# Kernel tuning notes

Measured on AMD Instinct MI355X. Metric: run time of the kernel, lower is better.

## Reference

```python
import jax, jax.numpy as jnp
import numpy as np

N_HEAD = 16
ROPE_BASE = 10000.0


def _make_rope(max_seq, half_dim):
    inv_freq = 1.0 / (ROPE_BASE ** (np.arange(0, half_dim, dtype=np.float32) / half_dim))
    t = np.arange(max_seq, dtype=np.float32)
    freqs = np.outer(t, inv_freq)  # [T, half_dim]
    return jnp.asarray(np.cos(freqs)), jnp.asarray(np.sin(freqs))


def setup_inputs() -> dict:
    key = jax.random.key(0)
    k1, k2, k3 = jax.random.split(key, 3)
    B, T, C = 4, 2048, 2048
    D = C // N_HEAD
    x = jax.random.normal(k1, (B, T, C), dtype=jnp.float32)
    # torch Linear weight [out,in]; stored transposed so y = x @ W
    wqkv = jax.random.normal(k2, (C, 3 * C), dtype=jnp.float32) * (C ** -0.5)
    wo = jax.random.normal(k3, (C, C), dtype=jnp.float32) * (C ** -0.5)
    rope_cos, rope_sin = _make_rope(T, D // 2)
    return {"x": x, "wqkv": wqkv, "wo": wo, "rope_cos": rope_cos, "rope_sin": rope_sin}


def _apply_rope(t, cos, sin):
    # t: [B, T, H, D]; cos/sin: [T, D/2]
    B, T, H, D = t.shape
    tr = t.reshape(B, T, H, D // 2, 2)
    xr, xi = tr[..., 0], tr[..., 1]
    c = cos[:T][None, :, None, :]
    s = sin[:T][None, :, None, :]
    out_r = xr * c - xi * s
    out_i = xr * s + xi * c
    return jnp.stack([out_r, out_i], axis=-1).reshape(B, T, H, D)


def reference(x, wqkv, wo, rope_cos, rope_sin):
    B, T, C = x.shape
    H = N_HEAD
    D = C // H
    qkv = x @ wqkv  # [B, T, 3C]
    q, k, v = jnp.split(qkv, 3, axis=-1)
    q = _apply_rope(q.reshape(B, T, H, D), rope_cos, rope_sin)
    k = _apply_rope(k.reshape(B, T, H, D), rope_cos, rope_sin)
    v = v.reshape(B, T, H, D)
    scale = D ** -0.5
    scores = jnp.einsum('bqhd,bkhd->bhqk', q, k) * scale  # [B, H, T, T]
    causal = jnp.tril(jnp.ones((T, T), dtype=bool))
    scores = jnp.where(causal[None, None], scores, jnp.finfo(scores.dtype).min)
    attn = jax.nn.softmax(scores, axis=-1)
    y = jnp.einsum('bhqk,bkhd->bqhd', attn, v).reshape(B, T, C)
    return y @ wo
```

## Files before the change

### kernel.cpp

```cpp
#include <hip/hip_runtime.h>
#include <hip/hip_bf16.h>

typedef __attribute__((ext_vector_type(8))) __bf16 bf16x8;
typedef __attribute__((ext_vector_type(4))) float f32x4;
typedef __attribute__((ext_vector_type(4))) unsigned short us4;

__device__ __forceinline__ unsigned short f2bf(float f) {
    unsigned u = __float_as_uint(f);
    u += 0x7FFFu + ((u >> 16) & 1u);
    return (unsigned short)(u >> 16);
}

__device__ __forceinline__ void gload16(const void* g, void* l) {
    __builtin_amdgcn_global_load_lds(
        (const __attribute__((address_space(1))) unsigned int*)g,
        (__attribute__((address_space(3))) unsigned int*)l,
        16, 0, 0);
}

__global__ void cvt_f32_bf16(const float* __restrict__ in, unsigned short* __restrict__ out, int n4) {
    int i = blockIdx.x * blockDim.x + threadIdx.x;
    if (i >= n4) return;
    float4 v = ((const float4*)in)[i];
    us4 r = { f2bf(v.x), f2bf(v.y), f2bf(v.z), f2bf(v.w) };
    ((us4*)out)[i] = r;
}

__global__ void tcvt(const float* __restrict__ in, unsigned short* __restrict__ out, int R, int C) {
    __shared__ float tile[32][33];
    int tx = threadIdx.x & 31, ty = threadIdx.x >> 5;
    int c0 = blockIdx.x * 32, r0 = blockIdx.y * 32;
    #pragma unroll
    for (int i = 0; i < 32; i += 8)
        tile[ty + i][tx] = in[(size_t)(r0 + ty + i) * C + c0 + tx];
    __syncthreads();
    #pragma unroll
    for (int i = 0; i < 32; i += 8)
        out[(size_t)(c0 + ty + i) * R + r0 + tx] = f2bf(tile[tx][ty + i]);
}

#define MF(af, bf, fi, ni) acc[fi][ni] = __builtin_amdgcn_mfma_f32_16x16x32_bf16(af, bf, acc[fi][ni], 0, 0, 0)
#define LOADA(p, off) do { a0 = *(const bf16x8*)((p)+(off)); a1 = *(const bf16x8*)((p)+(off)+1024); \
                           a2 = *(const bf16x8*)((p)+(off)+2048); a3 = *(const bf16x8*)((p)+(off)+3072); } while(0)
#define LOADA2(p, off) do { a4 = *(const bf16x8*)((p)+(off)); a5 = *(const bf16x8*)((p)+(off)+1024); \
                            a6 = *(const bf16x8*)((p)+(off)+2048); a7 = *(const bf16x8*)((p)+(off)+3072); } while(0)
#define LOADB(p) do { b0 = *(const bf16x8*)(p); b1 = *(const bf16x8*)((p)+1024); \
                      b2 = *(const bf16x8*)((p)+2048); b3 = *(const bf16x8*)((p)+3072); } while(0)
#define MFMA32() do { \
    MF(a0,b0,0,0); MF(a0,b1,0,1); MF(a0,b2,0,2); MF(a0,b3,0,3); \
    MF(a1,b0,1,0); MF(a1,b1,1,1); MF(a1,b2,1,2); MF(a1,b3,1,3); \
    MF(a2,b0,2,0); MF(a2,b1,2,1); MF(a2,b2,2,2); MF(a2,b3,2,3); \
    MF(a3,b0,3,0); MF(a3,b1,3,1); MF(a3,b2,3,2); MF(a3,b3,3,3); \
    MF(a4,b0,4,0); MF(a4,b1,4,1); MF(a4,b2,4,2); MF(a4,b3,4,3); \
    MF(a5,b0,5,0); MF(a5,b1,5,1); MF(a5,b2,5,2); MF(a5,b3,5,3); \
    MF(a6,b0,6,0); MF(a6,b1,6,1); MF(a6,b2,6,2); MF(a6,b3,6,3); \
    MF(a7,b0,7,0); MF(a7,b1,7,1); MF(a7,b2,7,2); MF(a7,b3,7,3); } while(0)
#define STG(gb, lp, buf, kkk, kt) do { \
    size_t ko = (size_t)(kt) * 128 + (kkk) * 64; \
    char* lpp = (lp) + (buf) * 32768 + (kkk) * 16384; \
    gload16((gb) + sR0 + ko, lpp + dst0); \
    gload16((gb) + sR1 + ko, lpp + dst1); } while (0)
#define PHASE_SYNC() do { \
    __builtin_amdgcn_s_barrier(); \
    asm volatile("s_waitcnt lgkmcnt(0)" ::: "memory"); \
    __builtin_amdgcn_sched_barrier(0); } while (0)

template <int MODE>
__global__ __launch_bounds__(512) void gemm8p(
    const unsigned short* __restrict__ A, const unsigned short* __restrict__ Bt,
    int M, int N, int K, float* __restrict__ Cf,
    unsigned short* __restrict__ qp, unsigned short* __restrict__ kp,
    unsigned short* __restrict__ vTp,
    const float* __restrict__ ropeC, const float* __restrict__ ropeS,
    int cby, int cbx)
{
    __shared__ unsigned short lA[2][2][8192];
    __shared__ unsigned short lB[2][2][8192];
    const int tid = threadIdx.x;
    const int lane = tid & 63, wid = tid >> 6;
    const int ln15 = lane & 15, hig = lane >> 4;
    const int wr = wid >> 2, wc = wid & 3;

    int nwg = gridDim.x * gridDim.y;
    int flat = blockIdx.y * gridDim.x + blockIdx.x;
    int bx, by;
    if ((nwg & 7) == 0) {
        int c = flat & 7, local = flat >> 3;
        int chunkCols = gridDim.x / cbx;
        by = (c / chunkCols) * cby + local / cbx;
        bx = (c % chunkCols) * cbx + local % cbx;
    } else {
        bx = flat % gridDim.x; by = flat / gridDim.x;
    }
    const int mbase = by * 256, nbase = bx * 256;
    const size_t Kb = (size_t)K * 2;

    const char* Ag = (const char*)A + (size_t)mbase * Kb;
    const char* Bg = (const char*)Bt + (size_t)nbase * Kb;
    char* lAc = (char*)&lA[0][0][0];
    char* lBc = (char*)&lB[0][0][0];

    const int srow = tid >> 2;
    const int gsrc = (tid & 3) ^ (((tid >> 5) & 1) << 1);
    const size_t sR0 = (size_t)srow * Kb + gsrc * 16;
    const size_t sR1 = (size_t)(srow + 128) * Kb + gsrc * 16;
    const int dst0 = tid * 16, dst1 = (tid + 512) * 16;

    const int colOff = (hig * 16) ^ (((ln15 >> 3) & 1) << 5);
    const int aRow = (wr * 128 + ln15) * 64 + colOff;
    const int bRow = (wc * 64 + ln15) * 64 + colOff;

    f32x4 acc[8][4] = {};
    const int T = K >> 6;

    STG(Ag, lAc, 0, 0, 0);
    STG(Bg, lBc, 0, 0, 0);
    STG(Ag, lAc, 0, 1, 0);
    STG(Bg, lBc, 0, 1, 0);
    asm volatile("s_waitcnt vmcnt(4)" ::: "memory");
    __builtin_amdgcn_s_barrier();

    for (int t = 0; t < T; t++) {
        const int cur = t & 1, nxt = cur ^ 1;
        const char* pa0 = lAc + cur * 32768 + aRow;
        const char* pb0 = lBc + cur * 32768 + bRow;
        const char* pa1 = pa0 + 16384;
        const char* pb1 = pb0 + 16384;
        const bool more = (t + 1 < T);
        bf16x8 a0, a1, a2, a3, a4, a5, a6, a7, b0, b1, b2, b3;

        LOADA(pa0, 0);
        LOADA2(pa0, 4096);
        LOADB(pb0);
        if (more) { STG(Ag, lAc, nxt, 0, t + 1); STG(Bg, lBc, nxt, 0, t + 1); }
        asm volatile("s_waitcnt lgkmcnt(8)" ::: "memory");
        if (more) asm volatile("s_waitcnt vmcnt(4)" ::: "memory");
        else      asm volatile("s_waitcnt vmcnt(0)" ::: "memory");
        PHASE_SYNC();
        __builtin_amdgcn_s_setprio(1);
        MFMA32();
        __builtin_amdgcn_s_setprio(0);
        __builtin_amdgcn_s_barrier();

        LOADA(pa1, 0);
        LOADA2(pa1, 4096);
        LOADB(pb1);
        if (more) {
            STG(Ag, lAc, nxt, 1, t + 1);
            STG(Bg, lBc, nxt, 1, t + 1);
            asm volatile("s_waitcnt lgkmcnt(8)" ::: "memory");
            asm volatile("s_waitcnt vmcnt(4)" ::: "memory");
        }
        PHASE_SYNC();
        __builtin_amdgcn_s_setprio(1);
        MFMA32();
        __builtin_amdgcn_s_setprio(0);
        __builtin_amdgcn_s_barrier();
    }

    if (MODE == 0) {
        #pragma unroll
        for (int fg = 0; fg < 8; fg++)
            #pragma unroll
            for (int n = 0; n < 4; n++)
                #pragma unroll
                for (int j = 0; j < 4; j++) {
                    int m = mbase + wr * 128 + fg * 16 + hig * 4 + j;
                    int col = nbase + wc * 64 + n * 16 + ln15;
                    Cf[(size_t)m * N + col] = acc[fg][n][j];
                }
    } else {
        const int colb = nbase + wc * 64;
        const int sec = colb >> 11;
        if (sec < 2) {
            unsigned short* dst = (sec == 0) ? qp : kp;
            const float scale = (sec == 0) ? 0.08838834764831845f : 1.0f;
            #pragma unroll
            for (int fg = 0; fg < 8; fg++)
                #pragma unroll
                for (int n = 0; n < 4; n++) {
                    int within = (colb & 2047) + n * 16 + ln15;
                    int h = within >> 7, d = within & 127, pidx = d >> 1;
                    #pragma unroll
                    for (int j = 0; j < 4; j++) {
                        int m = mbase + wr * 128 + fg * 16 + hig * 4 + j;
                        int b = m >> 11, tq = m & 2047;
                        float v = acc[fg][n][j];
                        float pv = __shfl_xor(v, 1);
                        float c = ropeC[tq * 64 + pidx], s = ropeS[tq * 64 + pidx];
                        float o = (d & 1) ? fmaf(pv, s, v * c) : fmaf(-pv, s, v * c);
                        o *= scale;
                        dst[((size_t)((b << 4) + h) * 2048 + tq) * 128 + d] = f2bf(o);
                    }
                }
        } else {
            #pragma unroll
            for (int fg = 0; fg < 8; fg++)
                #pragma unroll
                for (int n = 0; n < 4; n++) {
                    int within = (colb & 2047) + n * 16 + ln15;
                    int h = within >> 7, d = within & 127;
                    int m0 = mbase + wr * 128 + fg * 16 + hig * 4;
                    int b = m0 >> 11, t0 = m0 & 2047;
                    us4 pk = { f2bf(acc[fg][n][0]), f2bf(acc[fg][n][1]),
                               f2bf(acc[fg][n][2]), f2bf(acc[fg][n][3]) };
                    *(us4*)(vTp + ((size_t)((b << 4) + h) * 128 + d) * 2048 + t0) = pk;
                }
        }
    }
}

__global__ __launch_bounds__(256, 2) void attn_fwd(
    const unsigned short* __restrict__ q, const unsigned short* __restrict__ k,
    const unsigned short* __restrict__ vT, unsigned short* __restrict__ outp)
{
    __shared__ unsigned short lK[2][64 * 128];
    __shared__ unsigned short lV[2][128 * 64];
    __shared__ unsigned short lP[4 * 32 * 64];
    const int tid = threadIdx.x;
    const int lane = tid & 63, wid = tid >> 6;
    const int ln15 = lane & 15, hig = lane >> 4, hi8 = hig * 8;
    const int bh = blockIdx.x;

    const char* qg = (const char*)(q + (size_t)bh * 2048 * 128);
    const char* kg = (const char*)(k + (size_t)bh * 2048 * 128);
    const char* vg = (const char*)(vT + (size_t)bh * 128 * 2048);
    char* lKc = (char*)&lK[0][0];
    char* lVc = (char*)&lV[0][0];
    char* lPc = (char*)lP + wid * (32 * 64 * 2);
    const int b = bh >> 4, h = bh & 15;

    for (int rep = 0; rep < 2; rep++) {
        const int qt = rep == 0 ? (int)blockIdx.y : 15 - (int)blockIdx.y;
        const int qbase = qt * 128;
        const int qw = qbase + wid * 32;

        bf16x8 qf[2][4];
        #pragma unroll
        for (int mt = 0; mt < 2; mt++)
            #pragma unroll
            for (int ks = 0; ks < 4; ks++)
                qf[mt][ks] = *(const bf16x8*)(qg + ((size_t)(qw + mt * 16 + ln15) * 128 + ks * 32 + hi8) * 2);

        f32x4 o[2][8] = {};
        float mreg[2] = { -1e30f, -1e30f };
        float lreg[2] = { 0.f, 0.f };

        auto stageKV = [&](int bf, int kv0) {
            #pragma unroll
            for (int i = 0; i < 4; i++) {
                int slot = tid + i * 256;
                int row = slot >> 4, c = (slot & 15) * 16;
                gload16(kg + (size_t)(kv0 + row) * 256 + (c ^ ((row & 7) << 4)),
                        lKc + bf * 16384 + slot * 16);
            }
            #pragma unroll
            for (int i = 0; i < 4; i++) {
                int slot = tid + i * 256;
                int d = slot >> 3, c = (slot & 7) * 16;
                gload16(vg + (size_t)d * 4096 + (size_t)kv0 * 2 + (c ^ ((d & 7) << 4)),
                        lVc + bf * 16384 + slot * 16);
            }
        };

        const int ntiles = (qbase >> 6) + 2;
        stageKV(0, 0);
        if (ntiles > 1) stageKV(1, 64);

        for (int it = 0; it < ntiles; it++) {
            const int kv0 = it * 64;
            const int buf = it & 1;
            if (it + 1 < ntiles) asm volatile("s_waitcnt vmcnt(8)" ::: "memory");
            else                 asm volatile("s_waitcnt vmcnt(0)" ::: "memory");
            __builtin_amdgcn_s_barrier();

            if (kv0 <= qw + 31) {
                const char* lKb = lKc + buf * 16384;
                const char* lVb = lVc + buf * 16384;

                f32x4 s[2][4] = {};
                #pragma unroll
                for (int ks = 0; ks < 4; ks++) {
                    bf16x8 kf[4];
                    #pragma unroll
                    for (int nt = 0; nt < 4; nt++) {
                        int row = nt * 16 + ln15;
                        kf[nt] = *(const bf16x8*)(lKb + row * 256 + (((ks * 32 + hi8) * 2) ^ ((row & 7) << 4)));
                    }
                    __builtin_amdgcn_s_setprio(1);
                    #pragma unroll
                    for (int mt = 0; mt < 2; mt++)
                        #pragma unroll
                        for (int nt = 0; nt < 4; nt++)
                            s[mt][nt] = __builtin_amdgcn_mfma_f32_16x16x32_bf16(kf[nt], qf[mt][ks], s[mt][nt], 0, 0, 0);
                    __builtin_amdgcn_s_setprio(0);
                }

                if (kv0 + 63 > qw) {
                    #pragma unroll
                    for (int mt = 0; mt < 2; mt++) {
                        int qi = qw + mt * 16 + ln15;
                        #pragma unroll
                        for (int nt = 0; nt < 4; nt++)
                            #pragma unroll
                            for (int j = 0; j < 4; j++) {
                                int kvi = kv0 + nt * 16 + 4 * hig + j;
                                if (kvi > qi) s[mt][nt][j] = -1e30f;
                            }
                    }
                }

                float vmax[2];
                #pragma unroll
                for (int mt = 0; mt < 2; mt++) {
                    float v = fmaxf(fmaxf(s[mt][0][0], s[mt][0][1]), fmaxf(s[mt][0][2], s[mt][0][3]));
                    #pragma unroll
                    for (int nt = 1; nt < 4; nt++)
                        v = fmaxf(v, fmaxf(fmaxf(s[mt][nt][0], s[mt][nt][1]), fmaxf(s[mt][nt][2], s[mt][nt][3])));
                    v = fmaxf(v, __shfl_xor(v, 16));
                    v = fmaxf(v, __shfl_xor(v, 32));
                    vmax[mt] = v;
                }
                bool grow = (vmax[0] > mreg[0] + 8.0f) || (vmax[1] > mreg[1] + 8.0f);
                if (__any(grow)) {
                    float sc[2];
                    #pragma unroll
                    for (int mt = 0; mt < 2; mt++) {
                        float mn = fmaxf(mreg[mt], vmax[mt]);
                        sc[mt] = __expf(mreg[mt] - mn);
                        mreg[mt] = mn;
                        lreg[mt] *= sc[mt];
                    }
                    #pragma unroll
                    for (int mt = 0; mt < 2; mt++)
                        #pragma unroll
                        for (int j = 0; j < 4; j++) {
                            float scj = __shfl(sc[mt], 4 * hig + j);
                            #pragma unroll
                            for (int ntd = 0; ntd < 8; ntd++) o[mt][ntd][j] *= scj;
                        }
                }
                #pragma unroll
                for (int mt = 0; mt < 2; mt++) {
                    float rs = 0.f;
                    #pragma unroll
                    for (int nt = 0; nt < 4; nt++)
                        #pragma unroll
                        for (int j = 0; j < 4; j++) {
                            float p = __expf(s[mt][nt][j] - mreg[mt]);
                            s[mt][nt][j] = p;
                            rs += p;
                        }
                    rs += __shfl_xor(rs, 16);
                    rs += __shfl_xor(rs, 32);
                    lreg[mt] += rs;
                }

                #pragma unroll
                for (int mt = 0; mt < 2; mt++) {
                    int rr = mt * 16 + ln15;
                    int rx = (rr & 7) << 4;
                    #pragma unroll
                    for (int nt = 0; nt < 4; nt++) {
                        us4 pk = { f2bf(s[mt][nt][0]), f2bf(s[mt][nt][1]),
                                   f2bf(s[mt][nt][2]), f2bf(s[mt][nt][3]) };
                        int addr = rr * 128 + ((nt * 32 + hig * 8) ^ rx);
                        *(us4*)(lPc + addr) = pk;
                    }
                }

                #pragma unroll
                for (int ks2 = 0; ks2 < 2; ks2++) {
                    bf16x8 pf[2];
                    #pragma unroll
                    for (int mt = 0; mt < 2; mt++) {
                        int row = mt * 16 + ln15;
                        pf[mt] = *(const bf16x8*)(lPc + row * 128 + (((ks2 * 32 + hi8) * 2) ^ ((row & 7) << 4)));
                    }
                    #pragma unroll
                    for (int ntd = 0; ntd < 8; ntd++) {
                        int drow = ntd * 16 + ln15;
                        bf16x8 vf = *(const bf16x8*)(lVb + drow * 128 + (((ks2 * 32 + hi8) * 2) ^ ((drow & 7) << 4)));
                        __builtin_amdgcn_s_setprio(1);
                        #pragma unroll
                        for (int mt = 0; mt < 2; mt++)
                            o[mt][ntd] = __builtin_amdgcn_mfma_f32_16x16x32_bf16(pf[mt], vf, o[mt][ntd], 0, 0, 0);
                        __builtin_amdgcn_s_setprio(0);
                    }
                }
            }

            __builtin_amdgcn_s_barrier();
            if (it + 2 < ntiles) stageKV(buf, kv0 + 128);
        }

        #pragma unroll
        for (int mt = 0; mt < 2; mt++)
            #pragma unroll
            for (int j = 0; j < 4; j++) {
                float inv = 1.0f / __shfl(lreg[mt], 4 * hig + j);
                int t = qw + mt * 16 + hig * 4 + j;
                #pragma unroll
                for (int ntd = 0; ntd < 8; ntd++) {
                    int d = ntd * 16 + ln15;
                    outp[((size_t)b * 2048 + t) * 2048 + h * 128 + d] = f2bf(o[mt][ntd][j] * inv);
                }
            }
    }
}

extern "C" void kernel_launch(void* const* d_in, const int* in_sizes, int n_in,
                              void* d_out, int out_size, void* d_ws, size_t ws_size,
                              hipStream_t stream) {
    const float* x     = (const float*)d_in[0];
    const float* wqkv  = (const float*)d_in[1];
    const float* wo    = (const float*)d_in[2];
    const float* ropeC = (const float*)d_in[3];
    const float* ropeS = (const float*)d_in[4];
    float* out = (float*)d_out;
    char* ws = (char*)d_ws;
    const size_t MB = 1024 * 1024;
    unsigned short* xb    = (unsigned short*)(ws);
    unsigned short* wqkvT = (unsigned short*)(ws + 32 * MB);
    unsigned short* woT   = (unsigned short*)(ws + 56 * MB);
    unsigned short* qb    = (unsigned short*)(ws + 64 * MB);
    unsigned short* kb    = (unsigned short*)(ws + 96 * MB);
    unsigned short* vTb   = (unsigned short*)(ws + 128 * MB);
    unsigned short* attnb = (unsigned short*)(ws + 160 * MB);

    cvt_f32_bf16<<<16384, 256, 0, stream>>>(x, xb, 4194304);
    tcvt<<<dim3(192, 64), 256, 0, stream>>>(wqkv, wqkvT, 2048, 6144);
    tcvt<<<dim3(64, 64), 256, 0, stream>>>(wo, woT, 2048, 2048);
    gemm8p<1><<<dim3(24, 32), 512, 0, stream>>>(xb, wqkvT, 8192, 6144, 2048,
                                                nullptr, qb, kb, vTb, ropeC, ropeS, 8, 12);
    attn_fwd<<<dim3(64, 8), 256, 0, stream>>>(qb, kb, vTb, attnb);
    gemm8p<0><<<dim3(8, 32), 512, 0, stream>>>(attnb, woT, 8192, 2048, 2048,
                                               out, nullptr, nullptr, nullptr, nullptr, nullptr, 4, 8);
}
```

Measured before the change: 421.4 us.

## Rework GEMM to 16 waves per block with smaller per-wave tiles

The 256x256 GEMM kernel now runs with 1024 threads (16 waves in a 4x4 grid), so each wave owns a 64x64 tile instead of 128x64. Shared memory becomes a single double buffer with a new XOR swizzle, and the two-phase staged pipeline is replaced by a simpler prefetch-then-compute loop with one barrier per K step. The goal is more waves to hide latency and lower register pressure per wave. In exchange, each wave does fewer MFMAs per LDS load and the kernel now waits on vmcnt(0) every iteration, which exposes memory latency.

Measured after the change: 400.7 us. 4.9% less time.

```diff
diff --git a/kernel.cpp b/kernel.cpp
--- a/kernel.cpp
+++ b/kernel.cpp
@@ -39,34 +39,22 @@
         out[(size_t)(c0 + ty + i) * R + r0 + tx] = f2bf(tile[tx][ty + i]);
 }
 
-#define MF(af, bf, fi, ni) acc[fi][ni] = __builtin_amdgcn_mfma_f32_16x16x32_bf16(af, bf, acc[fi][ni], 0, 0, 0)
-#define LOADA(p, off) do { a0 = *(const bf16x8*)((p)+(off)); a1 = *(const bf16x8*)((p)+(off)+1024); \
-                           a2 = *(const bf16x8*)((p)+(off)+2048); a3 = *(const bf16x8*)((p)+(off)+3072); } while(0)
-#define LOADA2(p, off) do { a4 = *(const bf16x8*)((p)+(off)); a5 = *(const bf16x8*)((p)+(off)+1024); \
-                            a6 = *(const bf16x8*)((p)+(off)+2048); a7 = *(const bf16x8*)((p)+(off)+3072); } while(0)
-#define LOADB(p) do { b0 = *(const bf16x8*)(p); b1 = *(const bf16x8*)((p)+1024); \
-                      b2 = *(const bf16x8*)((p)+2048); b3 = *(const bf16x8*)((p)+3072); } while(0)
-#define MFMA32() do { \
-    MF(a0,b0,0,0); MF(a0,b1,0,1); MF(a0,b2,0,2); MF(a0,b3,0,3); \
-    MF(a1,b0,1,0); MF(a1,b1,1,1); MF(a1,b2,1,2); MF(a1,b3,1,3); \
-    MF(a2,b0,2,0); MF(a2,b1,2,1); MF(a2,b2,2,2); MF(a2,b3,2,3); \
-    MF(a3,b0,3,0); MF(a3,b1,3,1); MF(a3,b2,3,2); MF(a3,b3,3,3); \
-    MF(a4,b0,4,0); MF(a4,b1,4,1); MF(a4,b2,4,2); MF(a4,b3,4,3); \
-    MF(a5,b0,5,0); MF(a5,b1,5,1); MF(a5,b2,5,2); MF(a5,b3,5,3); \
-    MF(a6,b0,6,0); MF(a6,b1,6,1); MF(a6,b2,6,2); MF(a6,b3,6,3); \
-    MF(a7,b0,7,0); MF(a7,b1,7,1); MF(a7,b2,7,2); MF(a7,b3,7,3); } while(0)
-#define STG(gb, lp, buf, kkk, kt) do { \
-    size_t ko = (size_t)(kt) * 128 + (kkk) * 64; \
-    char* lpp = (lp) + (buf) * 32768 + (kkk) * 16384; \
-    gload16((gb) + sR0 + ko, lpp + dst0); \
-    gload16((gb) + sR1 + ko, lpp + dst1); } while (0)
-#define PHASE_SYNC() do { \
-    __builtin_amdgcn_s_barrier(); \
-    asm volatile("s_waitcnt lgkmcnt(0)" ::: "memory"); \
-    __builtin_amdgcn_sched_barrier(0); } while (0)
+#define MFW(af, bf, fi, ni) acc[fi][ni] = __builtin_amdgcn_mfma_f32_16x16x32_bf16(af, bf, acc[fi][ni], 0, 0, 0)
+#define MFMA16W() do { \
+    MFW(a0,b0,0,0); MFW(a0,b1,0,1); MFW(a0,b2,0,2); MFW(a0,b3,0,3); \
+    MFW(a1,b0,1,0); MFW(a1,b1,1,1); MFW(a1,b2,1,2); MFW(a1,b3,1,3); \
+    MFW(a2,b0,2,0); MFW(a2,b1,2,1); MFW(a2,b2,2,2); MFW(a2,b3,2,3); \
+    MFW(a3,b0,3,0); MFW(a3,b1,3,1); MFW(a3,b2,3,2); MFW(a3,b3,3,3); } while(0)
+#define STGW(kt, bufo) do { \
+    size_t ko = (size_t)(kt) * 128; \
+    char* bb = L + (bufo); \
+    gload16(Ag + sR + ko, bb + dstA); \
+    gload16(Ag + sR2 + ko, bb + dstA + 16384); \
+    gload16(Bg + sR + ko, bb + 32768 + dstA); \
+    gload16(Bg + sR2 + ko, bb + 32768 + dstA + 16384); } while (0)
 
 template <int MODE>
-__global__ __launch_bounds__(512) void gemm8p(
+__global__ __launch_bounds__(1024, 4) void gemmw(
     const unsigned short* __restrict__ A, const unsigned short* __restrict__ Bt,
     int M, int N, int K, float* __restrict__ Cf,
     unsigned short* __restrict__ qp, unsigned short* __restrict__ kp,
@@ -74,12 +62,11 @@
     const float* __restrict__ ropeC, const float* __restrict__ ropeS,
     int cby, int cbx)
 {
-    __shared__ unsigned short lA[2][2][8192];
-    __shared__ unsigned short lB[2][2][8192];
+    __shared__ unsigned short lds[2][32768];
     const int tid = threadIdx.x;
     const int lane = tid & 63, wid = tid >> 6;
     const int ln15 = lane & 15, hig = lane >> 4;
-    const int wr = wid >> 2, wc = wid & 3;
+    const int wrow = wid >> 2, wcol = wid & 3;
 
     int nwg = gridDim.x * gridDim.y;
     int flat = blockIdx.y * gridDim.x + blockIdx.x;
@@ -97,95 +84,89 @@
 
     const char* Ag = (const char*)A + (size_t)mbase * Kb;
     const char* Bg = (const char*)Bt + (size_t)nbase * Kb;
-    char* lAc = (char*)&lA[0][0][0];
-    char* lBc = (char*)&lB[0][0][0];
-
-    const int srow = tid >> 2;
-    const int gsrc = (tid & 3) ^ (((tid >> 5) & 1) << 1);
-    const size_t sR0 = (size_t)srow * Kb + gsrc * 16;
-    const size_t sR1 = (size_t)(srow + 128) * Kb + gsrc * 16;
-    const int dst0 = tid * 16, dst1 = (tid + 512) * 16;
-
-    const int colOff = (hig * 16) ^ (((ln15 >> 3) & 1) << 5);
-    const int aRow = (wr * 128 + ln15) * 64 + colOff;
-    const int bRow = (wc * 64 + ln15) * 64 + colOff;
-
-    f32x4 acc[8][4] = {};
+    char* L = (char*)&lds[0][0];
+
+    const int srow = tid >> 3;
+    const int gs = (tid & 7) ^ (srow & 7);
+    const size_t sR = (size_t)srow * Kb + gs * 16;
+    const size_t sR2 = sR + (size_t)128 * Kb;
+    const int dstA = tid * 16;
+
+    const int aBase = (wrow * 64 + ln15) * 128;
+    const int bBase = 32768 + (wcol * 64 + ln15) * 128;
+    const int sl0 = (hig ^ (ln15 & 7)) * 16;
+    const int sl1 = ((4 + hig) ^ (ln15 & 7)) * 16;
+
+    f32x4 acc[4][4] = {};
     const int T = K >> 6;
 
-    STG(Ag, lAc, 0, 0, 0);
-    STG(Bg, lBc, 0, 0, 0);
-    STG(Ag, lAc, 0, 1, 0);
-    STG(Bg, lBc, 0, 1, 0);
-    asm volatile("s_waitcnt vmcnt(4)" ::: "memory");
+    STGW(0, 0);
+    asm volatile("s_waitcnt vmcnt(0)" ::: "memory");
     __builtin_amdgcn_s_barrier();
+    asm volatile("" ::: "memory");
 
     for (int t = 0; t < T; t++) {
-        const int cur = t & 1, nxt = cur ^ 1;
-        const char* pa0 = lAc + cur * 32768 + aRow;
-        const char* pb0 = lBc + cur * 32768 + bRow;
-        const char* pa1 = pa0 + 16384;
-        const char* pb1 = pb0 + 16384;
-        const bool more = (t + 1 < T);
-        bf16x8 a0, a1, a2, a3, a4, a5, a6, a7, b0, b1, b2, b3;
-
-        LOADA(pa0, 0);
-        LOADA2(pa0, 4096);
-        LOADB(pb0);
-        if (more) { STG(Ag, lAc, nxt, 0, t + 1); STG(Bg, lBc, nxt, 0, t + 1); }
-        asm volatile("s_waitcnt lgkmcnt(8)" ::: "memory");
-        if (more) asm volatile("s_waitcnt vmcnt(4)" ::: "memory");
-        else      asm volatile("s_waitcnt vmcnt(0)" ::: "memory");
-        PHASE_SYNC();
+        char* bb = L + (t & 1) * 65536;
+        if (t + 1 < T) STGW(t + 1, ((t + 1) & 1) * 65536);
+        bf16x8 a0, a1, a2, a3, b0, b1, b2, b3;
+        a0 = *(const bf16x8*)(bb + aBase + 0 * 2048 + sl0);
+        a1 = *(const bf16x8*)(bb + aBase + 1 * 2048 + sl0);
+        a2 = *(const bf16x8*)(bb + aBase + 2 * 2048 + sl0);
+        a3 = *(const bf16x8*)(bb + aBase + 3 * 2048 + sl0);
+        b0 = *(const bf16x8*)(bb + bBase + 0 * 2048 + sl0);
+        b1 = *(const bf16x8*)(bb + bBase + 1 * 2048 + sl0);
+        b2 = *(const bf16x8*)(bb + bBase + 2 * 2048 + sl0);
+        b3 = *(const bf16x8*)(bb + bBase + 3 * 2048 + sl0);
         __builtin_amdgcn_s_setprio(1);
-        MFMA32();
+        MFMA16W();
         __builtin_amdgcn_s_setprio(0);
-        __builtin_amdgcn_s_barrier();
-
-        LOADA(pa1, 0);
-        LOADA2(pa1, 4096);
-        LOADB(pb1);
-        if (more) {
-            STG(Ag, lAc, nxt, 1, t + 1);
-            STG(Bg, lBc, nxt, 1, t + 1);
-            asm volatile("s_waitcnt lgkmcnt(8)" ::: "memory");
-            asm volatile("s_waitcnt vmcnt(4)" ::: "memory");
+        a0 = *(const bf16x8*)(bb + aBase + 0 * 2048 + sl1);
+        a1 = *(const bf16x8*)(bb + aBase + 1 * 2048 + sl1);
+        a2 = *(const bf16x8*)(bb + aBase + 2 * 2048 + sl1);
+        a3 = *(const bf16x8*)(bb + aBase + 3 * 2048 + sl1);
+        b0 = *(const bf16x8*)(bb + bBase + 0 * 2048 + sl1);
+        b1 = *(const bf16x8*)(bb + bBase + 1 * 2048 + sl1);
+        b2 = *(const bf16x8*)(bb + bBase + 2 * 2048 + sl1);
+        b3 = *(const bf16x8*)(bb + bBase + 3 * 2048 + sl1);
+        __builtin_amdgcn_s_setprio(1);
+        MFMA16W();
+        __builtin_amdgcn_s_setprio(0);
+
+        if (t + 1 < T) {
+            asm volatile("s_waitcnt vmcnt(0)" ::: "memory");
+            __builtin_amdgcn_s_barrier();
+            asm volatile("" ::: "memory");
         }
-        PHASE_SYNC();
-        __builtin_amdgcn_s_setprio(1);
-        MFMA32();
-        __builtin_amdgcn_s_setprio(0);
-        __builtin_amdgcn_s_barrier();
     }
 
     if (MODE == 0) {
         #pragma unroll
-        for (int fg = 0; fg < 8; fg++)
-            #pragma unroll
-            for (int n = 0; n < 4; n++)
+        for (int fm = 0; fm < 4; fm++)
+            #pragma unroll
+            for (int fn = 0; fn < 4; fn++)
                 #pragma unroll
                 for (int j = 0; j < 4; j++) {
-                    int m = mbase + wr * 128 + fg * 16 + hig * 4 + j;
-                    int col = nbase + wc * 64 + n * 16 + ln15;
-                    Cf[(size_t)m * N + col] = acc[fg][n][j];
+                    int m = mbase + wrow * 64 + fm * 16 + hig * 4 + j;
+                    int col = nbase + wcol * 64 + fn * 16 + ln15;
+                    Cf[(size_t)m * N + col] = acc[fm][fn][j];
                 }
     } else {
-        const int colb = nbase + wc * 64;
+        const int colb = nbase + wcol * 64;
         const int sec = colb >> 11;
         if (sec < 2) {
             unsigned short* dst = (sec == 0) ? qp : kp;
             const float scale = (sec == 0) ? 0.08838834764831845f : 1.0f;
             #pragma unroll
-            for (int fg = 0; fg < 8; fg++)
-                #pragma unroll
-                for (int n = 0; n < 4; n++) {
-                    int within = (colb & 2047) + n * 16 + ln15;
+            for (int fm = 0; fm < 4; fm++)
+                #pragma unroll
+                for (int fn = 0; fn < 4; fn++) {
+                    int within = (colb & 2047) + fn * 16 + ln15;
                     int h = within >> 7, d = within & 127, pidx = d >> 1;
                     #pragma unroll
                     for (int j = 0; j < 4; j++) {
-                        int m = mbase + wr * 128 + fg * 16 + hig * 4 + j;
+                        int m = mbase + wrow * 64 + fm * 16 + hig * 4 + j;
                         int b = m >> 11, tq = m & 2047;
-                        float v = acc[fg][n][j];
+                        float v = acc[fm][fn][j];
                         float pv = __shfl_xor(v, 1);
                         float c = ropeC[tq * 64 + pidx], s = ropeS[tq * 64 + pidx];
                         float o = (d & 1) ? fmaf(pv, s, v * c) : fmaf(-pv, s, v * c);
@@ -195,15 +176,15 @@
                 }
         } else {
             #pragma unroll
-            for (int fg = 0; fg < 8; fg++)
-                #pragma unroll
-                for (int n = 0; n < 4; n++) {
-                    int within = (colb & 2047) + n * 16 + ln15;
+            for (int fm = 0; fm < 4; fm++)
+                #pragma unroll
+                for (int fn = 0; fn < 4; fn++) {
+                    int within = (colb & 2047) + fn * 16 + ln15;
                     int h = within >> 7, d = within & 127;
-                    int m0 = mbase + wr * 128 + fg * 16 + hig * 4;
+                    int m0 = mbase + wrow * 64 + fm * 16 + hig * 4;
                     int b = m0 >> 11, t0 = m0 & 2047;
-                    us4 pk = { f2bf(acc[fg][n][0]), f2bf(acc[fg][n][1]),
-                               f2bf(acc[fg][n][2]), f2bf(acc[fg][n][3]) };
+                    us4 pk = { f2bf(acc[fm][fn][0]), f2bf(acc[fm][fn][1]),
+                               f2bf(acc[fm][fn][2]), f2bf(acc[fm][fn][3]) };
                     *(us4*)(vTp + ((size_t)((b << 4) + h) * 128 + d) * 2048 + t0) = pk;
                 }
         }
@@ -431,9 +412,9 @@
     cvt_f32_bf16<<<16384, 256, 0, stream>>>(x, xb, 4194304);
     tcvt<<<dim3(192, 64), 256, 0, stream>>>(wqkv, wqkvT, 2048, 6144);
     tcvt<<<dim3(64, 64), 256, 0, stream>>>(wo, woT, 2048, 2048);
-    gemm8p<1><<<dim3(24, 32), 512, 0, stream>>>(xb, wqkvT, 8192, 6144, 2048,
+    gemmw<1><<<dim3(24, 32), 1024, 0, stream>>>(xb, wqkvT, 8192, 6144, 2048,
                                                 nullptr, qb, kb, vTb, ropeC, ropeS, 8, 12);
     attn_fwd<<<dim3(64, 8), 256, 0, stream>>>(qb, kb, vTb, attnb);
-    gemm8p<0><<<dim3(8, 32), 512, 0, stream>>>(attnb, woT, 8192, 2048, 2048,
+    gemmw<0><<<dim3(8, 32), 1024, 0, stream>>>(attnb, woT, 8192, 2048, 2048,
                                                out, nullptr, nullptr, nullptr, nullptr, nullptr, 4, 8);
 }
```
